# Kernel optimization log

Measured on AMD Instinct MI355X. Metric: run time of the kernel, lower is better.

The kernel has to match this reference:

```python
import jax, jax.numpy as jnp
import numpy as np

N = 50000   # nodes
E = 800000  # edges per metapath
P = 3       # num_meta_paths
H = 4       # heads
D = 64      # out_size per head
IN = H * D  # in_size = 256 (required by residual g_emb.flatten(1) + h)
EPS = 1e-5
NEG_SLOPE = 0.2  # DGL GATConv leaky_relu default


def setup_inputs() -> dict:
    key = jax.random.key(0)
    ks = jax.random.split(key, 7)
    h = jax.random.normal(ks[0], (N, IN), jnp.float32)
    path_mask = jnp.ones((N, P), jnp.float32)
    src = jax.random.randint(ks[1], (P, E), 0, N, jnp.int32)
    dst = jax.random.randint(ks[2], (P, E), 0, N, jnp.int32)
    # per-metapath GATConv params (bias=False)
    fc_w = jax.random.normal(ks[3], (P, IN, H * D), jnp.float32) * 0.05
    attn_l = jax.random.normal(ks[4], (P, H, D), jnp.float32) * 0.05
    attn_r = jax.random.normal(ks[5], (P, H, D), jnp.float32) * 0.05
    bn_gamma = jnp.ones((IN,), jnp.float32)
    bn_beta = jnp.zeros((IN,), jnp.float32)
    return {"h": h, "path_mask": path_mask, "src": src, "dst": dst,
            "fc_w": fc_w, "attn_l": attn_l, "attn_r": attn_r,
            "bn_gamma": bn_gamma, "bn_beta": bn_beta}


def _gat(h, src, dst, w, al, ar):
    # DGL GATConv: linear proj, additive attention, edge-softmax over dst neighborhoods
    feat = (h @ w).reshape(N, H, D)                       # [N,H,D]
    el = jnp.sum(feat * al, axis=-1)                      # [N,H]
    er = jnp.sum(feat * ar, axis=-1)                      # [N,H]
    e = jax.nn.leaky_relu(el[src] + er[dst], NEG_SLOPE)   # [E,H]
    # numerically-stable segment softmax over incoming edges of each dst node
    m = jax.ops.segment_max(e, dst, num_segments=N)       # [N,H]
    ex = jnp.exp(e - m[dst])
    denom = jax.ops.segment_sum(ex, dst, num_segments=N)  # [N,H]
    alpha = ex / denom[dst]                               # [E,H]
    out = jax.ops.segment_sum(alpha[:, :, None] * feat[src], dst, num_segments=N)  # [N,H,D]
    return jax.nn.relu(out), alpha


def _bn(x, gamma, beta):
    # BatchNorm1d in training mode: batch statistics over node dim
    mu = jnp.mean(x, axis=0)
    var = jnp.var(x, axis=0)
    return gamma * (x - mu) * jax.lax.rsqrt(var + EPS) + beta


def reference(h, path_mask, src, dst, fc_w, attn_l, attn_r, bn_gamma, bn_beta):
    embs, attns = [], []
    for p in range(P):
        o, a = _gat(h, src[p], dst[p], fc_w[p], attn_l[p], attn_r[p])
        embs.append(_bn(o.reshape(N, H * D) + h, bn_gamma, bn_beta))
        attns.append(jnp.mean(a, axis=1))  # mean over heads -> per-edge coef [E]
    sem = jnp.stack(embs, axis=1)                              # [N,P,IN]
    w = path_mask / jnp.sum(path_mask, axis=1, keepdims=True)  # masked mean weights [N,P]
    pooled = jnp.einsum('np,npd->nd', w, sem)                  # [N,IN]
    gat_attns = jnp.stack(attns)                               # [P,E] (sparse values; indices = src/dst)
    return pooled, w, gat_attns
```

## Files before the change

### kernel.cpp

```cpp
#include <hip/hip_runtime.h>
#include <stdint.h>

#define N_NODES 50000
#define N_EDGES 800000
#define N_PATHS 3
#define N_HEADS 4
#define IN_F 256
#define BN_EPS 1e-5f
#define NEG_SLOPE 0.2f
#define CAP 48
#define NB_PER_PATH 49
#define NB_TOT (N_PATHS * NB_PER_PATH)
#define REC_CAP 18432
#define BIN_EPB 4096
#define TOT_EDGES (N_PATHS * N_EDGES)
#define BIN_BLOCKS ((TOT_EDGES + BIN_EPB - 1) / BIN_EPB)

typedef short bf16x8 __attribute__((ext_vector_type(8)));
typedef float f32x4 __attribute__((ext_vector_type(4)));

__device__ inline unsigned short f2bf(float f) {
  unsigned u = __float_as_uint(f);
  unsigned r = (u + 0x7FFFu + ((u >> 16) & 1u)) >> 16;
  return (unsigned short)r;
}
__device__ inline float bf2f(unsigned short s) {
  return __uint_as_float(((unsigned)s) << 16);
}
__device__ inline float bfl(unsigned u) { return __uint_as_float(u << 16); }
__device__ inline float bfh(unsigned u) { return __uint_as_float(u & 0xFFFF0000u); }

__global__ __launch_bounds__(256) void k_zero(unsigned* p, int nwords) {
  int i = blockIdx.x * 256 + threadIdx.x;
  if (i < nwords) p[i] = 0u;
}

__global__ __launch_bounds__(256) void k_convert_h(const float* __restrict__ h,
                                                   unsigned short* __restrict__ hbf) {
  int idx = (blockIdx.x * 256 + threadIdx.x) * 4;
  float4 v = *(const float4*)(h + idx);
  unsigned u0 = (unsigned)f2bf(v.x) | ((unsigned)f2bf(v.y) << 16);
  unsigned u1 = (unsigned)f2bf(v.z) | ((unsigned)f2bf(v.w) << 16);
  *(uint2*)(hbf + idx) = make_uint2(u0, u1);
}

__global__ __launch_bounds__(256) void k_convert_w(const float* __restrict__ fcw,
                                                   unsigned short* __restrict__ wbf) {
  __shared__ float sh[32][33];
  int bt = blockIdx.x;
  int p = bt >> 6;
  int tile = bt & 63;
  int tk = tile >> 3, tn = tile & 7;
  const float* base = fcw + (size_t)p * IN_F * IN_F;
  unsigned short* ob = wbf + (size_t)p * IN_F * IN_F;
  int c = threadIdx.x & 31, r0 = threadIdx.x >> 5;
  #pragma unroll
  for (int it = 0; it < 4; ++it) {
    int r = r0 + it * 8;
    sh[r][c] = base[(size_t)(tk * 32 + r) * IN_F + tn * 32 + c];
  }
  __syncthreads();
  #pragma unroll
  for (int it = 0; it < 4; ++it) {
    int r = r0 + it * 8;
    ob[(size_t)(tn * 32 + r) * IN_F + tk * 32 + c] = f2bf(sh[c][r]);
  }
}

__global__ __launch_bounds__(256) void k_wout(const float* __restrict__ pmask,
                                              float* __restrict__ wout) {
  int idx = blockIdx.x * 256 + threadIdx.x;
  if (idx >= N_NODES * N_PATHS) return;
  int n = idx / N_PATHS;
  float s = pmask[n * 3] + pmask[n * 3 + 1] + pmask[n * 3 + 2];
  wout[idx] = pmask[idx] / s;
}

__global__ __launch_bounds__(256) void k_bin(const int* __restrict__ src, const int* __restrict__ dst,
                                             unsigned* __restrict__ gcurP, unsigned* __restrict__ grec) {
  __shared__ unsigned hist[NB_TOT];
  __shared__ unsigned lbase[NB_TOT];
  __shared__ unsigned gbase[NB_TOT];
  __shared__ unsigned lcur[NB_TOT];
  __shared__ unsigned scanbuf[256];
  __shared__ unsigned char sbuck[BIN_EPB];
  __shared__ unsigned stage[BIN_EPB];
  int t = threadIdx.x;
  int base = blockIdx.x * BIN_EPB;
  for (int i = t; i < NB_TOT; i += 256) { hist[i] = 0u; lcur[i] = 0u; }
  __syncthreads();

  unsigned rec[16];
  int bk[16];
  #pragma unroll
  for (int k = 0; k < 16; ++k) {
    int gid = base + t + k * 256;
    bk[k] = -1;
    if (gid < TOT_EDGES) {
      int s = src[gid], d = dst[gid];
      int p = (gid >= 2 * N_EDGES) ? 2 : ((gid >= N_EDGES) ? 1 : 0);
      int b = p * NB_PER_PATH + (d >> 10);
      bk[k] = b;
      rec[k] = (unsigned)s | ((unsigned)(d & 1023) << 17);
      atomicAdd(&hist[b], 1u);
    }
  }
  __syncthreads();
  for (int i = t; i < NB_TOT; i += 256)
    gbase[i] = hist[i] ? atomicAdd(&gcurP[i * 16], hist[i]) : 0u;
  scanbuf[t] = (t < NB_TOT) ? hist[t] : 0u;
  __syncthreads();
  for (int off = 1; off < 256; off <<= 1) {
    unsigned v = (t >= off) ? scanbuf[t - off] : 0u;
    __syncthreads();
    scanbuf[t] += v;
    __syncthreads();
  }
  if (t < NB_TOT) lbase[t] = scanbuf[t] - hist[t];
  __syncthreads();
  #pragma unroll
  for (int k = 0; k < 16; ++k) {
    if (bk[k] >= 0) {
      int b = bk[k];
      unsigned pos = atomicAdd(&lcur[b], 1u) + lbase[b];
      stage[pos] = rec[k];
      sbuck[pos] = (unsigned char)b;
    }
  }
  __syncthreads();
  int nblk = TOT_EDGES - base;
  if (nblk > BIN_EPB) nblk = BIN_EPB;
  for (int i = t; i < nblk; i += 256) {
    int b = sbuck[i];
    unsigned off = (unsigned)i - lbase[b];
    unsigned gpos = gbase[b] + off;
    if (gpos < REC_CAP) grec[(size_t)b * REC_CAP + gpos] = stage[i];
  }
}

__global__ __launch_bounds__(1024) void k_fine(const unsigned* __restrict__ gcurP,
                                               const unsigned* __restrict__ grec,
                                               unsigned short* __restrict__ slots,
                                               int* __restrict__ cnt) {
  __shared__ unsigned cur[1024];
  int b = blockIdx.x;
  int p = b / NB_PER_PATH;
  int nb0 = (b % NB_PER_PATH) << 10;
  int t = threadIdx.x;
  cur[t] = 0u;
  __syncthreads();
  unsigned M = gcurP[b * 16];
  if (M > REC_CAP) M = REC_CAP;
  const unsigned* rb = grec + (size_t)b * REC_CAP;
  for (unsigned i = t; i < M; i += 1024) {
    unsigned r = rb[i];
    int node = r >> 17;
    int srcv = r & 0x1FFFF;
    unsigned pos = atomicAdd(&cur[node], 1u);
    if (pos < CAP)
      slots[((size_t)(p * N_NODES + nb0 + node)) * CAP + pos] = (unsigned short)srcv;
  }
  __syncthreads();
  int node = nb0 + t;
  if (node < N_NODES) cnt[p * N_NODES + node] = (int)cur[t];
}

__global__ __launch_bounds__(256) void k_gemm(const unsigned short* __restrict__ hbf,
                                              const unsigned short* __restrict__ wbf,
                                              const float* __restrict__ attl,
                                              const float* __restrict__ attr,
                                              unsigned short* __restrict__ featbf,
                                              float* __restrict__ el,
                                              float* __restrict__ erd) {
  __shared__ unsigned short As[64 * 264];
  __shared__ unsigned short Bs[64 * 264];
  __shared__ float sal[256];
  __shared__ float sar[256];
  int m0 = blockIdx.x * 64;
  int p = blockIdx.y;
  int tid = threadIdx.x;
  const unsigned short* wptr = wbf + (size_t)p * IN_F * IN_F;

  sal[tid] = attl[p * 256 + tid];
  sar[tid] = attr[p * 256 + tid];
  for (int i = tid; i < 2048; i += 256) {
    int r = i >> 5, g = i & 31;
    int gr = m0 + r;
    uint4 v = make_uint4(0, 0, 0, 0);
    if (gr < N_NODES) v = *(const uint4*)(hbf + (size_t)gr * IN_F + g * 8);
    *(uint4*)(&As[r * 264 + g * 8]) = v;
  }

  int wv = tid >> 6, lane = tid & 63;
  int l15 = lane & 15, quad = lane >> 4;
  const unsigned short* arow = &As[(wv * 16 + l15) * 264];
  size_t featbase = (size_t)p * N_NODES * IN_F;
  float* elp = el + (size_t)p * N_NODES * 4;
  float* erdp = erd + (size_t)p * N_NODES * 8;

  for (int c = 0; c < 4; ++c) {
    __syncthreads();
    for (int i = tid; i < 2048; i += 256) {
      int r = i >> 5, g = i & 31;
      *(uint4*)(&Bs[r * 264 + g * 8]) =
          *(const uint4*)(wptr + (size_t)(c * 64 + r) * IN_F + g * 8);
    }
    __syncthreads();

    f32x4 acc[4];
    #pragma unroll
    for (int i = 0; i < 4; ++i) acc[i] = (f32x4){0.f, 0.f, 0.f, 0.f};
    #pragma unroll
    for (int kb = 0; kb < 8; ++kb) {
      bf16x8 a = *(const bf16x8*)(arow + kb * 32 + quad * 8);
      #pragma unroll
      for (int nn = 0; nn < 4; ++nn) {
        bf16x8 b = *(const bf16x8*)(&Bs[(nn * 16 + l15) * 264 + kb * 32 + quad * 8]);
        acc[nn] = __builtin_amdgcn_mfma_f32_16x16x32_bf16(a, b, acc[nn], 0, 0, 0);
      }
    }
    #pragma unroll
    for (int nn = 0; nn < 4; ++nn)
      #pragma unroll
      for (int rg = 0; rg < 4; ++rg) {
        int grow = m0 + wv * 16 + quad * 4 + rg;
        if (grow < N_NODES)
          featbf[featbase + (size_t)grow * IN_F + c * 64 + nn * 16 + l15] = f2bf(acc[nn][rg]);
      }
    #pragma unroll
    for (int rg = 0; rg < 4; ++rg) {
      float a = 0.f, b = 0.f;
      #pragma unroll
      for (int nn = 0; nn < 4; ++nn) {
        float v = acc[nn][rg];
        int col = c * 64 + nn * 16 + l15;
        a += v * sal[col];
        b += v * sar[col];
      }
      a += __shfl_xor(a, 1); a += __shfl_xor(a, 2); a += __shfl_xor(a, 4); a += __shfl_xor(a, 8);
      b += __shfl_xor(b, 1); b += __shfl_xor(b, 2); b += __shfl_xor(b, 4); b += __shfl_xor(b, 8);
      int grow = m0 + wv * 16 + quad * 4 + rg;
      if (l15 == 0 && grow < N_NODES) {
        elp[(size_t)grow * 4 + c] = a;
        erdp[(size_t)grow * 8 + c] = b;
      }
    }
  }
}

__global__ __launch_bounds__(256) void k_gather(const int* __restrict__ cnt,
                                                const unsigned short* __restrict__ slots,
                                                const float* __restrict__ el,
                                                float* __restrict__ erd,
                                                const unsigned short* __restrict__ featbf,
                                                unsigned short* __restrict__ outbuf) {
  __shared__ float xs[4][4][CAP];
  __shared__ unsigned soff[4][CAP];
  int p = blockIdx.y;
  int tid = threadIdx.x;
  int wv = tid >> 6, lane = tid & 63;
  int node = blockIdx.x * 4 + wv;
  int b = p * N_NODES + node;
  int half = lane >> 5, lane32 = lane & 31;
  int head = lane32 >> 3;
  int m = cnt[b];
  if (m > CAP) m = CAP;
  const float* elp = el + (size_t)p * N_NODES * 4;
  float* erdp = erd + (size_t)p * N_NODES * 8;
  const unsigned short* sl = slots + (size_t)b * CAP;
  const char* fp_ = (const char*)featbf + (size_t)p * N_NODES * IN_F * 2 + lane32 * 16;

  {
    int headA = lane >> 4;
    float ern = erdp[(size_t)node * 8 + headA];
    for (int e = lane & 15; e < m; e += 16) {
      int s = (int)sl[e];
      if (headA == 0) soff[wv][e] = (unsigned)s * (unsigned)(IN_F * 2);
      float ev = elp[s * 4 + headA] + ern;
      ev = ev > 0.f ? ev : NEG_SLOPE * ev;
      xs[wv][headA][e] = __expf(ev);
    }
  }

  float a0 = 0.f, a1 = 0.f, a2 = 0.f, a3 = 0.f;
  float a4 = 0.f, a5 = 0.f, a6 = 0.f, a7 = 0.f, den = 0.f;
  int i = half;
  for (; i + 6 < m; i += 8) {
    unsigned o0 = soff[wv][i], o1 = soff[wv][i + 2], o2 = soff[wv][i + 4], o3 = soff[wv][i + 6];
    float x0 = xs[wv][head][i], x1 = xs[wv][head][i + 2];
    float x2 = xs[wv][head][i + 4], x3 = xs[wv][head][i + 6];
    uint4 f0 = *(const uint4*)(fp_ + o0);
    uint4 f1 = *(const uint4*)(fp_ + o1);
    uint4 f2 = *(const uint4*)(fp_ + o2);
    uint4 f3 = *(const uint4*)(fp_ + o3);
    den += (x0 + x1) + (x2 + x3);
    a0 += x0 * bfl(f0.x) + x1 * bfl(f1.x) + x2 * bfl(f2.x) + x3 * bfl(f3.x);
    a1 += x0 * bfh(f0.x) + x1 * bfh(f1.x) + x2 * bfh(f2.x) + x3 * bfh(f3.x);
    a2 += x0 * bfl(f0.y) + x1 * bfl(f1.y) + x2 * bfl(f2.y) + x3 * bfl(f3.y);
    a3 += x0 * bfh(f0.y) + x1 * bfh(f1.y) + x2 * bfh(f2.y) + x3 * bfh(f3.y);
    a4 += x0 * bfl(f0.z) + x1 * bfl(f1.z) + x2 * bfl(f2.z) + x3 * bfl(f3.z);
    a5 += x0 * bfh(f0.z) + x1 * bfh(f1.z) + x2 * bfh(f2.z) + x3 * bfh(f3.z);
    a6 += x0 * bfl(f0.w) + x1 * bfl(f1.w) + x2 * bfl(f2.w) + x3 * bfl(f3.w);
    a7 += x0 * bfh(f0.w) + x1 * bfh(f1.w) + x2 * bfh(f2.w) + x3 * bfh(f3.w);
  }
  for (; i + 2 < m; i += 4) {
    unsigned o0 = soff[wv][i], o1 = soff[wv][i + 2];
    float x0 = xs[wv][head][i], x1 = xs[wv][head][i + 2];
    uint4 f0 = *(const uint4*)(fp_ + o0);
    uint4 f1 = *(const uint4*)(fp_ + o1);
    den += x0 + x1;
    a0 += x0 * bfl(f0.x) + x1 * bfl(f1.x);
    a1 += x0 * bfh(f0.x) + x1 * bfh(f1.x);
    a2 += x0 * bfl(f0.y) + x1 * bfl(f1.y);
    a3 += x0 * bfh(f0.y) + x1 * bfh(f1.y);
    a4 += x0 * bfl(f0.z) + x1 * bfl(f1.z);
    a5 += x0 * bfh(f0.z) + x1 * bfh(f1.z);
    a6 += x0 * bfl(f0.w) + x1 * bfl(f1.w);
    a7 += x0 * bfh(f0.w) + x1 * bfh(f1.w);
  }
  for (; i < m; i += 2) {
    unsigned o0 = soff[wv][i];
    float x0 = xs[wv][head][i];
    uint4 f = *(const uint4*)(fp_ + o0);
    den += x0;
    a0 += x0 * bfl(f.x);
    a1 += x0 * bfh(f.x);
    a2 += x0 * bfl(f.y);
    a3 += x0 * bfh(f.y);
    a4 += x0 * bfl(f.z);
    a5 += x0 * bfh(f.z);
    a6 += x0 * bfl(f.w);
    a7 += x0 * bfh(f.w);
  }

  den += __shfl_xor(den, 32);
  a0 += __shfl_xor(a0, 32);
  a1 += __shfl_xor(a1, 32);
  a2 += __shfl_xor(a2, 32);
  a3 += __shfl_xor(a3, 32);
  a4 += __shfl_xor(a4, 32);
  a5 += __shfl_xor(a5, 32);
  a6 += __shfl_xor(a6, 32);
  a7 += __shfl_xor(a7, 32);
  if (half == 0) {
    float inv = den > 0.f ? 1.f / den : 0.f;
    float o0 = fmaxf(a0 * inv, 0.f), o1 = fmaxf(a1 * inv, 0.f);
    float o2 = fmaxf(a2 * inv, 0.f), o3 = fmaxf(a3 * inv, 0.f);
    float o4 = fmaxf(a4 * inv, 0.f), o5 = fmaxf(a5 * inv, 0.f);
    float o6 = fmaxf(a6 * inv, 0.f), o7 = fmaxf(a7 * inv, 0.f);
    uint4 u;
    u.x = (unsigned)f2bf(o0) | ((unsigned)f2bf(o1) << 16);
    u.y = (unsigned)f2bf(o2) | ((unsigned)f2bf(o3) << 16);
    u.z = (unsigned)f2bf(o4) | ((unsigned)f2bf(o5) << 16);
    u.w = (unsigned)f2bf(o6) | ((unsigned)f2bf(o7) << 16);
    *(uint4*)(outbuf + (size_t)b * IN_F + lane32 * 8) = u;
    if ((lane32 & 7) == 0) erdp[(size_t)node * 8 + 4 + head] = inv;
  }
}

__global__ __launch_bounds__(256) void k_attn(const int* __restrict__ src, const int* __restrict__ dst,
                                              const float* __restrict__ el,
                                              const float* __restrict__ erd,
                                              float* __restrict__ attn_out) {
  int eid = blockIdx.x * 256 + threadIdx.x;
  int p = eid / N_EDGES;
  int s = src[eid], t = dst[eid];
  const float* elp = el + (size_t)p * N_NODES * 4;
  const float* erdp = erd + (size_t)p * N_NODES * 8;
  float4 a = *(const float4*)(elp + (size_t)s * 4);
  float4 b = *(const float4*)(erdp + (size_t)t * 8);
  float4 idn = *(const float4*)(erdp + (size_t)t * 8 + 4);
  float4 e;
  e.x = a.x + b.x; e.x = e.x > 0.f ? e.x : NEG_SLOPE * e.x;
  e.y = a.y + b.y; e.y = e.y > 0.f ? e.y : NEG_SLOPE * e.y;
  e.z = a.z + b.z; e.z = e.z > 0.f ? e.z : NEG_SLOPE * e.z;
  e.w = a.w + b.w; e.w = e.w > 0.f ? e.w : NEG_SLOPE * e.w;
  attn_out[eid] = 0.25f * (__expf(e.x) * idn.x + __expf(e.y) * idn.y +
                           __expf(e.z) * idn.z + __expf(e.w) * idn.w);
}

__global__ __launch_bounds__(256) void k_bnstats3(const unsigned short* __restrict__ outbuf,
                                                  const float* __restrict__ h,
                                                  float* __restrict__ colsum, float* __restrict__ colsq) {
  int t = threadIdx.x;
  float s0 = 0.f, q0 = 0.f, s1 = 0.f, q1 = 0.f, s2 = 0.f, q2 = 0.f;
  for (int r = blockIdx.x; r < N_NODES; r += gridDim.x) {
    float hv = h[(size_t)r * IN_F + t];
    float v0 = bf2f(outbuf[(size_t)r * IN_F + t]) + hv;
    float v1 = bf2f(outbuf[((size_t)N_NODES + r) * IN_F + t]) + hv;
    float v2 = bf2f(outbuf[((size_t)2 * N_NODES + r) * IN_F + t]) + hv;
    s0 += v0; q0 += v0 * v0;
    s1 += v1; q1 += v1 * v1;
    s2 += v2; q2 += v2 * v2;
  }
  atomicAdd(&colsum[t], s0);
  atomicAdd(&colsq[t], q0);
  atomicAdd(&colsum[256 + t], s1);
  atomicAdd(&colsq[256 + t], q1);
  atomicAdd(&colsum[512 + t], s2);
  atomicAdd(&colsq[512 + t], q2);
}

__global__ __launch_bounds__(256) void k_bnapply3(const unsigned short* __restrict__ outbuf,
                                                  const float* __restrict__ h,
                                                  const float* __restrict__ colsum, const float* __restrict__ colsq,
                                                  const float* __restrict__ gamma, const float* __restrict__ beta,
                                                  const float* __restrict__ pmask,
                                                  float* __restrict__ pooled) {
  __shared__ float spm[3];
  int n = blockIdx.x, t = threadIdx.x;
  if (t < 3) spm[t] = pmask[n * 3 + t];
  __syncthreads();
  float ssum = spm[0] + spm[1] + spm[2];
  const float invN = 1.f / (float)N_NODES;
  float hv = h[(size_t)n * IN_F + t];
  float g = gamma[t], bt = beta[t];
  float pv = 0.f;
  #pragma unroll
  for (int p = 0; p < 3; ++p) {
    float mu = colsum[p * 256 + t] * invN;
    float var = colsq[p * 256 + t] * invN - mu * mu;
    float rs = rsqrtf(var + BN_EPS);
    float v = bf2f(outbuf[((size_t)p * N_NODES + n) * IN_F + t]) + hv;
    float emb = g * (v - mu) * rs + bt;
    pv += (spm[p] / ssum) * emb;
  }
  pooled[(size_t)n * IN_F + t] = pv;
}

extern "C" void kernel_launch(void* const* d_in, const int* in_sizes, int n_in,
                              void* d_out, int out_size, void* d_ws, size_t ws_size,
                              hipStream_t stream) {
  const float* h     = (const float*)d_in[0];
  const float* pmask = (const float*)d_in[1];
  const int*   src   = (const int*)d_in[2];
  const int*   dst   = (const int*)d_in[3];
  const float* fcw   = (const float*)d_in[4];
  const float* attl  = (const float*)d_in[5];
  const float* attr  = (const float*)d_in[6];
  const float* gamma = (const float*)d_in[7];
  const float* beta  = (const float*)d_in[8];

  float* out_pooled = (float*)d_out;
  float* out_w = out_pooled + (size_t)N_NODES * IN_F;
  float* out_attn = out_w + (size_t)N_NODES * N_PATHS;

  char* wp = (char*)d_ws;
  auto carve = [&](size_t bytes) {
    char* r = wp;
    wp += (bytes + 255) & ~(size_t)255;
    return r;
  };
  unsigned short* hbf    = (unsigned short*)carve((size_t)N_NODES * IN_F * 2);
  unsigned short* featbf = (unsigned short*)carve((size_t)N_PATHS * N_NODES * IN_F * 2);
  unsigned short* wbf    = (unsigned short*)carve((size_t)N_PATHS * IN_F * IN_F * 2);
  unsigned short* outbuf = (unsigned short*)carve((size_t)N_PATHS * N_NODES * IN_F * 2);
  char* grec_base = carve((size_t)NB_TOT * REC_CAP * 4);
  unsigned* grec = (unsigned*)grec_base;
  float* el  = (float*)grec_base;
  float* erd = el + (size_t)N_PATHS * N_NODES * 4;
  unsigned short* slots = (unsigned short*)carve((size_t)N_PATHS * N_NODES * CAP * 2);
  int* cnt = (int*)carve((size_t)N_PATHS * N_NODES * 4);
  char* zbase = wp;
  unsigned* gcurP = (unsigned*)carve((size_t)NB_TOT * 16 * 4);
  float* colsum = (float*)carve((size_t)N_PATHS * IN_F * 4);
  float* colsq  = (float*)carve((size_t)N_PATHS * IN_F * 4);
  int zero_words = (int)((wp - zbase) / 4);

  k_convert_h<<<(N_NODES * IN_F) / 1024, 256, 0, stream>>>(h, hbf);
  k_convert_w<<<N_PATHS * 64, 256, 0, stream>>>(fcw, wbf);
  k_wout<<<(N_NODES * N_PATHS + 255) / 256, 256, 0, stream>>>(pmask, out_w);
  k_zero<<<(zero_words + 255) / 256, 256, 0, stream>>>((unsigned*)zbase, zero_words);
  k_bin<<<BIN_BLOCKS, 256, 0, stream>>>(src, dst, gcurP, grec);
  k_fine<<<NB_TOT, 1024, 0, stream>>>(gcurP, grec, slots, cnt);
  k_gemm<<<dim3((N_NODES + 63) / 64, N_PATHS), 256, 0, stream>>>(hbf, wbf, attl, attr,
                                                                 featbf, el, erd);
  k_gather<<<dim3(N_NODES / 4, N_PATHS), 256, 0, stream>>>(cnt, slots, el, erd, featbf, outbuf);
  k_attn<<<TOT_EDGES / 256, 256, 0, stream>>>(src, dst, el, erd, out_attn);
  k_bnstats3<<<512, 256, 0, stream>>>(outbuf, h, colsum, colsq);
  k_bnapply3<<<N_NODES, 256, 0, stream>>>(outbuf, h, colsum, colsq, gamma, beta, pmask,
                                          out_pooled);
}
```

Baseline: 555.6 us.

## Replace two-pass bucketed CSR build with direct global-atomic slot insertion

Replaces the two-stage binning (block-local histogram, scan, bucket records, then per-bucket fine pass with shared atomics) with a single kernel that does a global atomicAdd per edge on the destination counter and writes the source straight into that node's slot array. It also folds the path-weight output into the BN apply kernel, removing one launch. Costs are 2.4M global atomics spread over 150K counters and scattered 2-byte writes, in exchange for dropping the intermediate record buffer and one kernel launch. el/erd now get their own buffers instead of aliasing the record buffer.

```diff
diff --git a/kernel.cpp b/kernel.cpp
--- a/kernel.cpp
+++ b/kernel.cpp
@@ -9,12 +9,7 @@
 #define BN_EPS 1e-5f
 #define NEG_SLOPE 0.2f
 #define CAP 48
-#define NB_PER_PATH 49
-#define NB_TOT (N_PATHS * NB_PER_PATH)
-#define REC_CAP 18432
-#define BIN_EPB 4096
 #define TOT_EDGES (N_PATHS * N_EDGES)
-#define BIN_BLOCKS ((TOT_EDGES + BIN_EPB - 1) / BIN_EPB)
 
 typedef short bf16x8 __attribute__((ext_vector_type(8)));
 typedef float f32x4 __attribute__((ext_vector_type(4)));
@@ -67,102 +62,17 @@
   }
 }
 
-__global__ __launch_bounds__(256) void k_wout(const float* __restrict__ pmask,
-                                              float* __restrict__ wout) {
-  int idx = blockIdx.x * 256 + threadIdx.x;
-  if (idx >= N_NODES * N_PATHS) return;
-  int n = idx / N_PATHS;
-  float s = pmask[n * 3] + pmask[n * 3 + 1] + pmask[n * 3 + 2];
-  wout[idx] = pmask[idx] / s;
-}
-
-__global__ __launch_bounds__(256) void k_bin(const int* __restrict__ src, const int* __restrict__ dst,
-                                             unsigned* __restrict__ gcurP, unsigned* __restrict__ grec) {
-  __shared__ unsigned hist[NB_TOT];
-  __shared__ unsigned lbase[NB_TOT];
-  __shared__ unsigned gbase[NB_TOT];
-  __shared__ unsigned lcur[NB_TOT];
-  __shared__ unsigned scanbuf[256];
-  __shared__ unsigned char sbuck[BIN_EPB];
-  __shared__ unsigned stage[BIN_EPB];
-  int t = threadIdx.x;
-  int base = blockIdx.x * BIN_EPB;
-  for (int i = t; i < NB_TOT; i += 256) { hist[i] = 0u; lcur[i] = 0u; }
-  __syncthreads();
-
-  unsigned rec[16];
-  int bk[16];
-  #pragma unroll
-  for (int k = 0; k < 16; ++k) {
-    int gid = base + t + k * 256;
-    bk[k] = -1;
-    if (gid < TOT_EDGES) {
-      int s = src[gid], d = dst[gid];
-      int p = (gid >= 2 * N_EDGES) ? 2 : ((gid >= N_EDGES) ? 1 : 0);
-      int b = p * NB_PER_PATH + (d >> 10);
-      bk[k] = b;
-      rec[k] = (unsigned)s | ((unsigned)(d & 1023) << 17);
-      atomicAdd(&hist[b], 1u);
-    }
-  }
-  __syncthreads();
-  for (int i = t; i < NB_TOT; i += 256)
-    gbase[i] = hist[i] ? atomicAdd(&gcurP[i * 16], hist[i]) : 0u;
-  scanbuf[t] = (t < NB_TOT) ? hist[t] : 0u;
-  __syncthreads();
-  for (int off = 1; off < 256; off <<= 1) {
-    unsigned v = (t >= off) ? scanbuf[t - off] : 0u;
-    __syncthreads();
-    scanbuf[t] += v;
-    __syncthreads();
-  }
-  if (t < NB_TOT) lbase[t] = scanbuf[t] - hist[t];
-  __syncthreads();
-  #pragma unroll
-  for (int k = 0; k < 16; ++k) {
-    if (bk[k] >= 0) {
-      int b = bk[k];
-      unsigned pos = atomicAdd(&lcur[b], 1u) + lbase[b];
-      stage[pos] = rec[k];
-      sbuck[pos] = (unsigned char)b;
-    }
-  }
-  __syncthreads();
-  int nblk = TOT_EDGES - base;
-  if (nblk > BIN_EPB) nblk = BIN_EPB;
-  for (int i = t; i < nblk; i += 256) {
-    int b = sbuck[i];
-    unsigned off = (unsigned)i - lbase[b];
-    unsigned gpos = gbase[b] + off;
-    if (gpos < REC_CAP) grec[(size_t)b * REC_CAP + gpos] = stage[i];
-  }
-}
-
-__global__ __launch_bounds__(1024) void k_fine(const unsigned* __restrict__ gcurP,
-                                               const unsigned* __restrict__ grec,
-                                               unsigned short* __restrict__ slots,
-                                               int* __restrict__ cnt) {
-  __shared__ unsigned cur[1024];
-  int b = blockIdx.x;
-  int p = b / NB_PER_PATH;
-  int nb0 = (b % NB_PER_PATH) << 10;
-  int t = threadIdx.x;
-  cur[t] = 0u;
-  __syncthreads();
-  unsigned M = gcurP[b * 16];
-  if (M > REC_CAP) M = REC_CAP;
-  const unsigned* rb = grec + (size_t)b * REC_CAP;
-  for (unsigned i = t; i < M; i += 1024) {
-    unsigned r = rb[i];
-    int node = r >> 17;
-    int srcv = r & 0x1FFFF;
-    unsigned pos = atomicAdd(&cur[node], 1u);
-    if (pos < CAP)
-      slots[((size_t)(p * N_NODES + nb0 + node)) * CAP + pos] = (unsigned short)srcv;
-  }
-  __syncthreads();
-  int node = nb0 + t;
-  if (node < N_NODES) cnt[p * N_NODES + node] = (int)cur[t];
+__global__ __launch_bounds__(256) void k_bin2(const int* __restrict__ src,
+                                              const int* __restrict__ dst,
+                                              int* __restrict__ cnt,
+                                              unsigned short* __restrict__ slots) {
+  int gid = blockIdx.x * 256 + threadIdx.x;
+  if (gid >= TOT_EDGES) return;
+  int s = src[gid], d = dst[gid];
+  int p = (gid >= 2 * N_EDGES) ? 2 : ((gid >= N_EDGES) ? 1 : 0);
+  int b = p * N_NODES + d;
+  int pos = atomicAdd(&cnt[b], 1);
+  if (pos < CAP) slots[(size_t)b * CAP + pos] = (unsigned short)s;
 }
 
 __global__ __launch_bounds__(256) void k_gemm(const unsigned short* __restrict__ hbf,
@@ -406,12 +316,14 @@
                                                   const float* __restrict__ colsum, const float* __restrict__ colsq,
                                                   const float* __restrict__ gamma, const float* __restrict__ beta,
                                                   const float* __restrict__ pmask,
-                                                  float* __restrict__ pooled) {
+                                                  float* __restrict__ pooled,
+                                                  float* __restrict__ wout) {
   __shared__ float spm[3];
   int n = blockIdx.x, t = threadIdx.x;
   if (t < 3) spm[t] = pmask[n * 3 + t];
   __syncthreads();
   float ssum = spm[0] + spm[1] + spm[2];
+  if (t < 3) wout[n * 3 + t] = spm[t] / ssum;
   const float invN = 1.f / (float)N_NODES;
   float hv = h[(size_t)n * IN_F + t];
   float g = gamma[t], bt = beta[t];
@@ -455,29 +367,24 @@
   unsigned short* featbf = (unsigned short*)carve((size_t)N_PATHS * N_NODES * IN_F * 2);
   unsigned short* wbf    = (unsigned short*)carve((size_t)N_PATHS * IN_F * IN_F * 2);
   unsigned short* outbuf = (unsigned short*)carve((size_t)N_PATHS * N_NODES * IN_F * 2);
-  char* grec_base = carve((size_t)NB_TOT * REC_CAP * 4);
-  unsigned* grec = (unsigned*)grec_base;
-  float* el  = (float*)grec_base;
-  float* erd = el + (size_t)N_PATHS * N_NODES * 4;
+  float* el  = (float*)carve((size_t)N_PATHS * N_NODES * 4 * 4);
+  float* erd = (float*)carve((size_t)N_PATHS * N_NODES * 8 * 4);
   unsigned short* slots = (unsigned short*)carve((size_t)N_PATHS * N_NODES * CAP * 2);
+  char* zbase = wp;
   int* cnt = (int*)carve((size_t)N_PATHS * N_NODES * 4);
-  char* zbase = wp;
-  unsigned* gcurP = (unsigned*)carve((size_t)NB_TOT * 16 * 4);
   float* colsum = (float*)carve((size_t)N_PATHS * IN_F * 4);
   float* colsq  = (float*)carve((size_t)N_PATHS * IN_F * 4);
   int zero_words = (int)((wp - zbase) / 4);
 
   k_convert_h<<<(N_NODES * IN_F) / 1024, 256, 0, stream>>>(h, hbf);
   k_convert_w<<<N_PATHS * 64, 256, 0, stream>>>(fcw, wbf);
-  k_wout<<<(N_NODES * N_PATHS + 255) / 256, 256, 0, stream>>>(pmask, out_w);
   k_zero<<<(zero_words + 255) / 256, 256, 0, stream>>>((unsigned*)zbase, zero_words);
-  k_bin<<<BIN_BLOCKS, 256, 0, stream>>>(src, dst, gcurP, grec);
-  k_fine<<<NB_TOT, 1024, 0, stream>>>(gcurP, grec, slots, cnt);
+  k_bin2<<<(TOT_EDGES + 255) / 256, 256, 0, stream>>>(src, dst, cnt, slots);
   k_gemm<<<dim3((N_NODES + 63) / 64, N_PATHS), 256, 0, stream>>>(hbf, wbf, attl, attr,
                                                                  featbf, el, erd);
   k_gather<<<dim3(N_NODES / 4, N_PATHS), 256, 0, stream>>>(cnt, slots, el, erd, featbf, outbuf);
   k_attn<<<TOT_EDGES / 256, 256, 0, stream>>>(src, dst, el, erd, out_attn);
   k_bnstats3<<<512, 256, 0, stream>>>(outbuf, h, colsum, colsq);
   k_bnapply3<<<N_NODES, 256, 0, stream>>>(outbuf, h, colsum, colsq, gamma, beta, pmask,
-                                          out_pooled);
-}
+                                          out_pooled, out_w);
+}
```

Result: slower. 685.3 us (+23.3%).

## Fuse per-edge attention output into gather by storing edge ids in slots

Applied to the files above, without the earlier changes.

Slots now hold edge ids instead of source node ids, so the gather kernel looks up src through the edge id and can write the head-averaged attention coefficient directly, scattered to the edge's output position. This removes the separate k_attn pass, which reread src/dst, el and erd and recomputed exponentials for every edge. The path-weight output is folded into the BN apply kernel, removing k_wout. In exchange, slot storage doubles to 32-bit, gather takes an extra dependent load through src, and the attention writes become scattered. Edges beyond CAP per node would get no attention value.

```diff
diff --git a/kernel.cpp b/kernel.cpp
--- a/kernel.cpp
+++ b/kernel.cpp
@@ -67,15 +67,6 @@
   }
 }
 
-__global__ __launch_bounds__(256) void k_wout(const float* __restrict__ pmask,
-                                              float* __restrict__ wout) {
-  int idx = blockIdx.x * 256 + threadIdx.x;
-  if (idx >= N_NODES * N_PATHS) return;
-  int n = idx / N_PATHS;
-  float s = pmask[n * 3] + pmask[n * 3 + 1] + pmask[n * 3 + 2];
-  wout[idx] = pmask[idx] / s;
-}
-
 __global__ __launch_bounds__(256) void k_bin(const int* __restrict__ src, const int* __restrict__ dst,
                                              unsigned* __restrict__ gcurP, unsigned* __restrict__ grec) {
   __shared__ unsigned hist[NB_TOT];
@@ -97,11 +88,12 @@
     int gid = base + t + k * 256;
     bk[k] = -1;
     if (gid < TOT_EDGES) {
-      int s = src[gid], d = dst[gid];
+      int d = dst[gid];
       int p = (gid >= 2 * N_EDGES) ? 2 : ((gid >= N_EDGES) ? 1 : 0);
       int b = p * NB_PER_PATH + (d >> 10);
       bk[k] = b;
-      rec[k] = (unsigned)s | ((unsigned)(d & 1023) << 17);
+      unsigned eid = (unsigned)(gid - p * N_EDGES);
+      rec[k] = ((unsigned)(d & 1023) << 22) | eid;
       atomicAdd(&hist[b], 1u);
     }
   }
@@ -140,7 +132,7 @@
 
 __global__ __launch_bounds__(1024) void k_fine(const unsigned* __restrict__ gcurP,
                                                const unsigned* __restrict__ grec,
-                                               unsigned short* __restrict__ slots,
+                                               unsigned* __restrict__ slots,
                                                int* __restrict__ cnt) {
   __shared__ unsigned cur[1024];
   int b = blockIdx.x;
@@ -154,11 +146,11 @@
   const unsigned* rb = grec + (size_t)b * REC_CAP;
   for (unsigned i = t; i < M; i += 1024) {
     unsigned r = rb[i];
-    int node = r >> 17;
-    int srcv = r & 0x1FFFF;
+    int node = r >> 22;
+    unsigned eid = r & 0x3FFFFFu;
     unsigned pos = atomicAdd(&cur[node], 1u);
     if (pos < CAP)
-      slots[((size_t)(p * N_NODES + nb0 + node)) * CAP + pos] = (unsigned short)srcv;
+      slots[((size_t)(p * N_NODES + nb0 + node)) * CAP + pos] = eid;
   }
   __syncthreads();
   int node = nb0 + t;
@@ -249,13 +241,17 @@
 }
 
 __global__ __launch_bounds__(256) void k_gather(const int* __restrict__ cnt,
-                                                const unsigned short* __restrict__ slots,
+                                                const unsigned* __restrict__ slots,
+                                                const int* __restrict__ src,
                                                 const float* __restrict__ el,
                                                 float* __restrict__ erd,
                                                 const unsigned short* __restrict__ featbf,
-                                                unsigned short* __restrict__ outbuf) {
+                                                unsigned short* __restrict__ outbuf,
+                                                float* __restrict__ attn_out) {
   __shared__ float xs[4][4][CAP];
   __shared__ unsigned soff[4][CAP];
+  __shared__ unsigned seid[4][CAP];
+  __shared__ float sinv[4][4];
   int p = blockIdx.y;
   int tid = threadIdx.x;
   int wv = tid >> 6, lane = tid & 63;
@@ -267,15 +263,17 @@
   if (m > CAP) m = CAP;
   const float* elp = el + (size_t)p * N_NODES * 4;
   float* erdp = erd + (size_t)p * N_NODES * 8;
-  const unsigned short* sl = slots + (size_t)b * CAP;
+  const unsigned* sl = slots + (size_t)b * CAP;
+  const int* srcp = src + (size_t)p * N_EDGES;
   const char* fp_ = (const char*)featbf + (size_t)p * N_NODES * IN_F * 2 + lane32 * 16;
 
   {
     int headA = lane >> 4;
     float ern = erdp[(size_t)node * 8 + headA];
     for (int e = lane & 15; e < m; e += 16) {
-      int s = (int)sl[e];
-      if (headA == 0) soff[wv][e] = (unsigned)s * (unsigned)(IN_F * 2);
+      unsigned eid = sl[e];
+      int s = srcp[eid];
+      if (headA == 0) { soff[wv][e] = (unsigned)s * (unsigned)(IN_F * 2); seid[wv][e] = eid; }
       float ev = elp[s * 4 + headA] + ern;
       ev = ev > 0.f ? ev : NEG_SLOPE * ev;
       xs[wv][headA][e] = __expf(ev);
@@ -342,8 +340,9 @@
   a5 += __shfl_xor(a5, 32);
   a6 += __shfl_xor(a6, 32);
   a7 += __shfl_xor(a7, 32);
+  float inv = den > 0.f ? 1.f / den : 0.f;
+  sinv[wv][head] = inv;
   if (half == 0) {
-    float inv = den > 0.f ? 1.f / den : 0.f;
     float o0 = fmaxf(a0 * inv, 0.f), o1 = fmaxf(a1 * inv, 0.f);
     float o2 = fmaxf(a2 * inv, 0.f), o3 = fmaxf(a3 * inv, 0.f);
     float o4 = fmaxf(a4 * inv, 0.f), o5 = fmaxf(a5 * inv, 0.f);
@@ -356,27 +355,12 @@
     *(uint4*)(outbuf + (size_t)b * IN_F + lane32 * 8) = u;
     if ((lane32 & 7) == 0) erdp[(size_t)node * 8 + 4 + head] = inv;
   }
-}
-
-__global__ __launch_bounds__(256) void k_attn(const int* __restrict__ src, const int* __restrict__ dst,
-                                              const float* __restrict__ el,
-                                              const float* __restrict__ erd,
-                                              float* __restrict__ attn_out) {
-  int eid = blockIdx.x * 256 + threadIdx.x;
-  int p = eid / N_EDGES;
-  int s = src[eid], t = dst[eid];
-  const float* elp = el + (size_t)p * N_NODES * 4;
-  const float* erdp = erd + (size_t)p * N_NODES * 8;
-  float4 a = *(const float4*)(elp + (size_t)s * 4);
-  float4 b = *(const float4*)(erdp + (size_t)t * 8);
-  float4 idn = *(const float4*)(erdp + (size_t)t * 8 + 4);
-  float4 e;
-  e.x = a.x + b.x; e.x = e.x > 0.f ? e.x : NEG_SLOPE * e.x;
-  e.y = a.y + b.y; e.y = e.y > 0.f ? e.y : NEG_SLOPE * e.y;
-  e.z = a.z + b.z; e.z = e.z > 0.f ? e.z : NEG_SLOPE * e.z;
-  e.w = a.w + b.w; e.w = e.w > 0.f ? e.w : NEG_SLOPE * e.w;
-  attn_out[eid] = 0.25f * (__expf(e.x) * idn.x + __expf(e.y) * idn.y +
-                           __expf(e.z) * idn.z + __expf(e.w) * idn.w);
+
+  for (int e = lane; e < m; e += 64) {
+    float am = 0.25f * (xs[wv][0][e] * sinv[wv][0] + xs[wv][1][e] * sinv[wv][1] +
+                        xs[wv][2][e] * sinv[wv][2] + xs[wv][3][e] * sinv[wv][3]);
+    attn_out[(size_t)p * N_EDGES + seid[wv][e]] = am;
+  }
 }
 
 __global__ __launch_bounds__(256) void k_bnstats3(const unsigned short* __restrict__ outbuf,
@@ -406,12 +390,14 @@
                                                   const float* __restrict__ colsum, const float* __restrict__ colsq,
                                                   const float* __restrict__ gamma, const float* __restrict__ beta,
                                                   const float* __restrict__ pmask,
-                                                  float* __restrict__ pooled) {
+                                                  float* __restrict__ pooled,
+                                                  float* __restrict__ wout) {
   __shared__ float spm[3];
   int n = blockIdx.x, t = threadIdx.x;
   if (t < 3) spm[t] = pmask[n * 3 + t];
   __syncthreads();
   float ssum = spm[0] + spm[1] + spm[2];
+  if (t < 3) wout[n * 3 + t] = spm[t] / ssum;
   const float invN = 1.f / (float)N_NODES;
   float hv = h[(size_t)n * IN_F + t];
   float g = gamma[t], bt = beta[t];
@@ -459,7 +445,7 @@
   unsigned* grec = (unsigned*)grec_base;
   float* el  = (float*)grec_base;
   float* erd = el + (size_t)N_PATHS * N_NODES * 4;
-  unsigned short* slots = (unsigned short*)carve((size_t)N_PATHS * N_NODES * CAP * 2);
+  unsigned* slots = (unsigned*)carve((size_t)N_PATHS * N_NODES * CAP * 4);
   int* cnt = (int*)carve((size_t)N_PATHS * N_NODES * 4);
   char* zbase = wp;
   unsigned* gcurP = (unsigned*)carve((size_t)NB_TOT * 16 * 4);
@@ -469,15 +455,14 @@
 
   k_convert_h<<<(N_NODES * IN_F) / 1024, 256, 0, stream>>>(h, hbf);
   k_convert_w<<<N_PATHS * 64, 256, 0, stream>>>(fcw, wbf);
-  k_wout<<<(N_NODES * N_PATHS + 255) / 256, 256, 0, stream>>>(pmask, out_w);
   k_zero<<<(zero_words + 255) / 256, 256, 0, stream>>>((unsigned*)zbase, zero_words);
   k_bin<<<BIN_BLOCKS, 256, 0, stream>>>(src, dst, gcurP, grec);
   k_fine<<<NB_TOT, 1024, 0, stream>>>(gcurP, grec, slots, cnt);
   k_gemm<<<dim3((N_NODES + 63) / 64, N_PATHS), 256, 0, stream>>>(hbf, wbf, attl, attr,
                                                                  featbf, el, erd);
-  k_gather<<<dim3(N_NODES / 4, N_PATHS), 256, 0, stream>>>(cnt, slots, el, erd, featbf, outbuf);
-  k_attn<<<TOT_EDGES / 256, 256, 0, stream>>>(src, dst, el, erd, out_attn);
+  k_gather<<<dim3(N_NODES / 4, N_PATHS), 256, 0, stream>>>(cnt, slots, src, el, erd,
+                                                           featbf, outbuf, out_attn);
   k_bnstats3<<<512, 256, 0, stream>>>(outbuf, h, colsum, colsq);
   k_bnapply3<<<N_NODES, 256, 0, stream>>>(outbuf, h, colsum, colsq, gamma, beta, pmask,
-                                          out_pooled);
-}
+                                          out_pooled, out_w);
+}
```

New measurement: 612.3 us. 10.2% more time.
